# Kernel tuning notes

Hardware: AMD Instinct MI355X
Metric: run time of the kernel (lower is better)

## Reference

```python
import jax, jax.numpy as jnp
import numpy as np

B, T, I, H, L, S = 128, 256, 256, 256, 4, 3


def _gru(x_t, w_i, b_i, b_h):
    # torch.nn.GRUCell called WITHOUT hx in the source => hidden state is 0,
    # so Whh @ 0 vanishes and only the b_hh bias contributes to the gates.
    gi = x_t @ w_i.T + b_i                      # [B, 3H]
    hh = b_h.shape[0] // 3
    i_r, i_z, i_n = gi[:, :hh], gi[:, hh:2 * hh], gi[:, 2 * hh:]
    h_r, h_z, h_n = b_h[:hh], b_h[hh:2 * hh], b_h[2 * hh:]
    r = jax.nn.sigmoid(i_r + h_r)
    z = jax.nn.sigmoid(i_z + h_z)
    n = jnp.tanh(i_n + r * h_n)
    return (1.0 - z) * n                        # + z * 0


def setup_inputs() -> dict:
    key = jax.random.key(0)
    ks = jax.random.split(key, 12)
    s = 1.0 / np.sqrt(H)
    u = lambda k, shape: jax.random.uniform(k, shape, jnp.float32, -s, s)
    return {
        "x": jax.random.normal(ks[0], (B, T, I), jnp.float32),
        "hidden": jax.random.normal(ks[1], (B, L, L), jnp.float32),
        "w_ih0": u(ks[2], (S, 3 * H, I)),      # layer-0 input weights, per split
        "b_ih0": u(ks[3], (S, 3 * H)),
        "b_hh0": u(ks[4], (S, 3 * H)),
        "w_ih": u(ks[5], (S, L - 1, 3 * H, H)),  # layers 1..L-1
        "b_ih": u(ks[6], (S, L - 1, 3 * H)),
        "b_hh": u(ks[7], (S, L - 1, 3 * H)),
        "w_lw": u(ks[8], (L, H)),              # layer_weights: Linear(H -> L)
        "b_lw": u(ks[9], (L,)),
        "w_sel": u(ks[10], (S, H + I)),        # selective_layer: Linear(H+I -> S)
        "b_sel": u(ks[11], (S,)),
    }


def reference(x, hidden, w_ih0, b_ih0, b_hh0, w_ih, b_ih, b_hh, w_lw, b_lw, w_sel, b_sel):
    Lm1 = w_ih.shape[1]

    def run_stack(x_t, cur):
        # cur is a (possibly traced) int index selecting one of S GRU stacks
        hs = [_gru(x_t, w_ih0[cur], b_ih0[cur], b_hh0[cur])]
        for l in range(Lm1):
            hs.append(_gru(hs[-1], w_ih[cur, l], b_ih[cur, l], b_hh[cur, l]))
        return jnp.stack(hs, axis=1)            # [B, L, H]

    h0 = run_stack(x[:, 0, :], 0)               # first step always uses stack 0

    def step(h, x_t):
        energy = h @ w_lw.T + b_lw              # [B, L, L]
        attn = jnp.sum(hidden * energy, axis=2) # [B, L]
        a = jax.nn.softmax(attn, axis=1)
        ctx = jnp.einsum('bl,blh->bh', a, h)    # [B, H]
        scores = jnp.concatenate([ctx, x_t], axis=1) @ w_sel.T + b_sel  # [B, S]
        cur = jnp.argmax(jnp.sum(scores, axis=0))  # batch-summed routing
        h_new = run_stack(x_t, cur)
        return h_new, h_new[:, -1, :]

    h_final, ys = jax.lax.scan(step, h0, jnp.swapaxes(x[:, 1:, :], 0, 1))
    outputs = jnp.concatenate([h0[:, -1:, :], jnp.swapaxes(ys, 0, 1)], axis=1)  # [B, T, H]
    return outputs, h_final[:, -1, :]
```

## Files before the change

### kernel.cpp

```cpp
#include <hip/hip_runtime.h>
#include <math.h>

#define Bsz 128
#define Tsz 256
#define Isz 256
#define Hsz 256
#define Lsz 4
#define Ssz 3
#define Mrows (Bsz*Tsz)

using f16x8 = __attribute__((ext_vector_type(8))) _Float16;
using f32x4 = __attribute__((ext_vector_type(4))) float;

#define LOG2E 1.44269504f

__global__ __launch_bounds__(256) void f32_to_f16_3(
    const float* __restrict__ s0, _Float16* __restrict__ d0, int n0,
    const float* __restrict__ s1, _Float16* __restrict__ d1, int n1,
    const float* __restrict__ s2, _Float16* __restrict__ d2, int n2)
{
  int idx = blockIdx.x * 256 + threadIdx.x;
  const float* s; _Float16* d;
  if (idx < n0)           { s = s0; d = d0; }
  else if (idx < n0 + n1) { idx -= n0; s = s1; d = d1; }
  else                    { idx -= n0 + n1; if (idx >= n2) return; s = s2; d = d2; }
  const float4 v0 = *(const float4*)(s + (size_t)idx * 8);
  const float4 v1 = *(const float4*)(s + (size_t)idx * 8 + 4);
  _Float16 h[8];
  h[0] = (_Float16)v0.x; h[1] = (_Float16)v0.y;
  h[2] = (_Float16)v0.z; h[3] = (_Float16)v0.w;
  h[4] = (_Float16)v1.x; h[5] = (_Float16)v1.y;
  h[6] = (_Float16)v1.z; h[7] = (_Float16)v1.w;
  *(uint4*)(d + (size_t)idx * 8) = *(uint4*)h;
}

__global__ __launch_bounds__(256, 2) void gemm_gru_f16(
    const _Float16* __restrict__ Abase, size_t a_cur_stride,
    const _Float16* __restrict__ Wbase, size_t w_cur_stride,
    const float* __restrict__ bi_g, size_t bi_stride,
    const float* __restrict__ bh_g, size_t bh_stride,
    _Float16* __restrict__ Hout)
{
  __shared__ _Float16 AhS[3][8192];

  const int tid  = threadIdx.x;
  const int cu   = blockIdx.z;
  const int n0   = blockIdx.y * 64;
  const int rmb  = blockIdx.x * 256;

  const _Float16* A = Abase + (size_t)cu * a_cur_stride;
  const _Float16* W = Wbase + (size_t)cu * w_cur_stride;
  const float* bi = bi_g + (size_t)cu * bi_stride;
  const float* bh = bh_g + (size_t)cu * bh_stride;

  const int lane = tid & 63;
  const int wv   = tid >> 6;
  const int q    = lane >> 4;
  const int c    = lane & 15;

  const int ncol = n0 + wv * 16 + c;
  f16x8 wf[3][8];
  #pragma unroll
  for (int s = 0; s < 3; s++)
    #pragma unroll
    for (int k0 = 0; k0 < 8; k0++)
      wf[s][k0] = *(const f16x8*)(W + (size_t)(s * 256 + ncol) * 256 + k0 * 32 + q * 8);
  #pragma unroll
  for (int s = 0; s < 3; s++)
    #pragma unroll
    for (int k0 = 0; k0 < 8; k0++)
      asm volatile("" : "+v"(wf[s][k0]));

  const float c0  = -LOG2E * (bi[ncol] + bh[ncol]);
  const float c1  =  LOG2E * (bi[256 + ncol] + bh[256 + ncol]);
  const float c3  = 2.f * LOG2E * bi[512 + ncol];
  const float bhn = bh[512 + ncol];

  f32x4 acc[3][2];

  auto stage = [&](int buf, int ch) {
    const int rm = rmb + ch * 32;
    #pragma unroll
    for (int i = 0; i < 4; i++) {
      const int p0 = 8 * wv + 2 * i;
      const int pk = p0 + (lane >> 5);
      const _Float16* src = A + (size_t)(rm + (lane & 31)) * 256 + pk * 8;
      __builtin_amdgcn_global_load_lds(
          (const __attribute__((address_space(1))) void*)src,
          (__attribute__((address_space(3))) void*)&AhS[buf][p0 * 256],
          16, 0, 0);
    }
  };

  auto compute_chunk = [&](int buf, int ch) {
    const int rm = rmb + ch * 32;
    #pragma unroll
    for (int s = 0; s < 3; s++)
      #pragma unroll
      for (int mi = 0; mi < 2; mi++)
        acc[s][mi] = (f32x4)0.f;
    #pragma unroll
    for (int k0 = 0; k0 < 8; k0++) {
      const f16x8 a0 = *(const f16x8*)&AhS[buf][(k0 * 4 + q) * 256 + c * 8];
      const f16x8 a1 = *(const f16x8*)&AhS[buf][(k0 * 4 + q) * 256 + 128 + c * 8];
      #pragma unroll
      for (int s = 0; s < 3; s++) {
        acc[s][0] = __builtin_amdgcn_mfma_f32_16x16x32_f16(a0, wf[s][k0], acc[s][0], 0, 0, 0);
        acc[s][1] = __builtin_amdgcn_mfma_f32_16x16x32_f16(a1, wf[s][k0], acc[s][1], 0, 0, 0);
      }
    }
    #pragma unroll
    for (int mi = 0; mi < 2; mi++) {
      #pragma unroll
      for (int reg = 0; reg < 4; reg++) {
        const float ar = acc[0][mi][reg];
        const float az = acc[1][mi][reg];
        const float an = acc[2][mi][reg];
        const float e0 = __builtin_amdgcn_exp2f(fmaf(-LOG2E, ar, c0));
        const float r  = __builtin_amdgcn_rcpf(1.f + e0);
        const float e1 = __builtin_amdgcn_exp2f(fmaf(LOG2E, az, c1));
        const float tt = fmaf(r, bhn, an);
        const float a2 = fminf(fmaf(2.f * LOG2E, tt, c3), 120.f);
        const float e2 = __builtin_amdgcn_exp2f(a2);
        const float out = (e2 - 1.f) *
            __builtin_amdgcn_rcpf((1.f + e1) * (1.f + e2));
        const size_t row = (size_t)cu * Mrows + rm + mi * 16 + q * 4 + reg;
        Hout[row * 256 + ncol] = (_Float16)out;
      }
    }
  };

  stage(0, 0);
  stage(1, 1);
  asm volatile("s_waitcnt vmcnt(4)" ::: "memory");
  __builtin_amdgcn_s_barrier();

  int bc = 0;
  for (int t = 0; t < 6; ++t) {
    int bs = bc + 2; if (bs >= 3) bs -= 3;
    stage(bs, t + 2);
    compute_chunk(bc, t);
    asm volatile("s_waitcnt vmcnt(12)" ::: "memory");
    __builtin_amdgcn_s_barrier();
    bc = (bc + 1 == 3) ? 0 : bc + 1;
  }
  compute_chunk(bc, 6);
  asm volatile("s_waitcnt vmcnt(0)" ::: "memory");
  __builtin_amdgcn_s_barrier();
  compute_chunk(1, 7);
}

__global__ __launch_bounds__(256) void ep_tile(
    const _Float16* __restrict__ Hh,
    const float* __restrict__ w_lw, const float* __restrict__ w_sel, int layer,
    float* __restrict__ e, float* __restrict__ p)
{
  __shared__ float wc[7][256];
  __shared__ float ps[4][64][8];
  const int tid = threadIdx.x;
  const size_t mg0 = (size_t)blockIdx.x * 64;

  #pragma unroll
  for (int j = 0; j < 7; j++)
    wc[j][tid] = (j < 4) ? w_lw[j * 256 + tid] : w_sel[(j - 4) * 512 + tid];
  __syncthreads();

  const int r = tid & 63, pp = tid >> 6;
  const _Float16* hrow = Hh + (mg0 + r) * 256 + pp * 64;
  float acc[7] = {0.f, 0.f, 0.f, 0.f, 0.f, 0.f, 0.f};
  #pragma unroll
  for (int i = 0; i < 8; i++) {
    union { uint4 u; _Float16 h[8]; } hv;
    hv.u = *(const uint4*)(hrow + i * 8);
    float hf[8];
    #pragma unroll
    for (int k = 0; k < 8; k++) hf[k] = (float)hv.h[k];
    #pragma unroll
    for (int j = 0; j < 7; j++) {
      const float4 w0 = *(const float4*)&wc[j][pp * 64 + i * 8];
      const float4 w1 = *(const float4*)&wc[j][pp * 64 + i * 8 + 4];
      acc[j] += hf[0] * w0.x + hf[1] * w0.y + hf[2] * w0.z + hf[3] * w0.w
              + hf[4] * w1.x + hf[5] * w1.y + hf[6] * w1.z + hf[7] * w1.w;
    }
  }
  #pragma unroll
  for (int j = 0; j < 7; j++) ps[pp][r][j] = acc[j];
  __syncthreads();

  if (tid < 64) {
    float d[7];
    #pragma unroll
    for (int j = 0; j < 7; j++)
      d[j] = ps[0][tid][j] + ps[1][tid][j] + ps[2][tid][j] + ps[3][tid][j];
    const size_t mg = mg0 + tid;
    const int cc = (int)(mg >> 15);
    const int m  = (int)(mg & 32767);
    const int b = m >> 8, t = m & 255;
    const size_t base = ((size_t)cc * Tsz + t) * Bsz + b;
    #pragma unroll
    for (int j = 0; j < 4; j++) e[base * 16 + layer * 4 + j] = d[j];
    #pragma unroll
    for (int j = 0; j < 3; j++) p[base * 12 + layer * 3 + j] = d[4 + j];
  }
}

__global__ __launch_bounds__(128) void attn_finish(
    const float* __restrict__ e, const float* __restrict__ p,
    const float* __restrict__ hidden, const float* __restrict__ b_lw,
    float* __restrict__ score_h)
{
  const int t = blockIdx.x, cc = blockIdx.y;
  const int b = threadIdx.x;
  const float* eb = e + ((size_t)(cc * Tsz + t) * Bsz + b) * 16;
  const float* pb = p + ((size_t)(cc * Tsz + t) * Bsz + b) * 12;
  const float* hb = hidden + b * 16;
  const float bl0 = b_lw[0], bl1 = b_lw[1], bl2 = b_lw[2], bl3 = b_lw[3];
  float attn[4];
  #pragma unroll
  for (int i = 0; i < 4; i++) {
    attn[i] = hb[i * 4 + 0] * (eb[i * 4 + 0] + bl0)
            + hb[i * 4 + 1] * (eb[i * 4 + 1] + bl1)
            + hb[i * 4 + 2] * (eb[i * 4 + 2] + bl2)
            + hb[i * 4 + 3] * (eb[i * 4 + 3] + bl3);
  }
  const float mx = fmaxf(fmaxf(attn[0], attn[1]), fmaxf(attn[2], attn[3]));
  float ex[4], sum = 0.f;
  #pragma unroll
  for (int i = 0; i < 4; i++) { ex[i] = expf(attn[i] - mx); sum += ex[i]; }
  const float inv = 1.f / sum;
  float sc[3];
  #pragma unroll
  for (int s = 0; s < 3; s++) {
    float v = 0.f;
    #pragma unroll
    for (int i = 0; i < 4; i++) v += ex[i] * pb[i * 3 + s];
    sc[s] = v * inv;
  }
  #pragma unroll
  for (int off = 32; off; off >>= 1)
    #pragma unroll
    for (int s = 0; s < 3; s++) sc[s] += __shfl_xor(sc[s], off);
  __shared__ float red[2][3];
  const int wv = threadIdx.x >> 6, ln = threadIdx.x & 63;
  if (ln == 0) { red[wv][0] = sc[0]; red[wv][1] = sc[1]; red[wv][2] = sc[2]; }
  __syncthreads();
  if (threadIdx.x == 0) {
    #pragma unroll
    for (int s = 0; s < 3; s++)
      score_h[((size_t)cc * Tsz + t) * 3 + s] = red[0][s] + red[1][s];
  }
}

__global__ __launch_bounds__(256) void xs_kernel(
    const float* __restrict__ x, const float* __restrict__ w_sel,
    const float* __restrict__ b_sel, float* __restrict__ xs)
{
  const int t = blockIdx.x, k = threadIdx.x;
  float s = 0.f;
  for (int b = 0; b < Bsz; b++) s += x[((size_t)b * Tsz + t) * Isz + k];
  float pr[3];
  #pragma unroll
  for (int qq = 0; qq < 3; qq++) pr[qq] = s * w_sel[qq * (Hsz + Isz) + Hsz + k];
  #pragma unroll
  for (int off = 32; off; off >>= 1)
    #pragma unroll
    for (int qq = 0; qq < 3; qq++) pr[qq] += __shfl_xor(pr[qq], off);
  __shared__ float red[4][3];
  const int wv = k >> 6, ln = k & 63;
  if (ln == 0) { red[wv][0] = pr[0]; red[wv][1] = pr[1]; red[wv][2] = pr[2]; }
  __syncthreads();
  if (k == 0) {
    #pragma unroll
    for (int qq = 0; qq < 3; qq++)
      xs[t * 3 + qq] = red[0][qq] + red[1][qq] + red[2][qq] + red[3][qq]
                      + (float)Bsz * b_sel[qq];
  }
}

__global__ __launch_bounds__(256) void select_kernel(
    const float* __restrict__ score_h, const float* __restrict__ xs,
    int* __restrict__ cur)
{
  __shared__ unsigned S[Tsz];
  const int t = threadIdx.x;

  unsigned m = 0x24;
  if (t >= 1) {
    m = 0;
    const float* xr = xs + t * 3;
    #pragma unroll
    for (int cc = 0; cc < 3; cc++) {
      const float* sh = score_h + ((size_t)cc * Tsz + (t - 1)) * 3;
      const float v0 = sh[0] + xr[0];
      const float v1 = sh[1] + xr[1];
      const float v2 = sh[2] + xr[2];
      unsigned best = 0; float bv = v0;
      if (v1 > bv) { bv = v1; best = 1; }
      if (v2 > bv) { bv = v2; best = 2; }
      m |= best << (2 * cc);
    }
  }
  S[t] = m;
  __syncthreads();

  #pragma unroll
  for (int d = 1; d < Tsz; d <<= 1) {
    const unsigned prev = (t >= d) ? S[t - d] : 0x24u;
    const unsigned self = S[t];
    __syncthreads();
    unsigned comp = 0;
    #pragma unroll
    for (int x = 0; x < 3; x++) {
      const unsigned y = (prev >> (2 * x)) & 3u;
      const unsigned z = (self >> (2 * y)) & 3u;
      comp |= z << (2 * x);
    }
    S[t] = comp;
    __syncthreads();
  }
  cur[t] = (int)(S[t] & 3u);
}

__global__ __launch_bounds__(256) void gather_out(
    const _Float16* __restrict__ Hh, const int* __restrict__ cur,
    float* __restrict__ out)
{
  const size_t idx = ((size_t)blockIdx.x * 256 + threadIdx.x) * 4;
  const size_t BTH = (size_t)Bsz * Tsz * Hsz;
  int b, t, h;
  if (idx < BTH) {
    b = (int)(idx >> 16);
    const int rem = (int)(idx & 65535);
    t = rem >> 8; h = rem & 255;
  } else {
    const size_t r2 = idx - BTH;
    b = (int)(r2 >> 8); h = (int)(r2 & 255); t = Tsz - 1;
  }
  const int cc = cur[t];
  const size_t g = (((size_t)cc * Mrows + (size_t)b * Tsz + t) * Hsz + h);
  union { ushort4 u; _Float16 hv[4]; } cv;
  cv.u = *(const ushort4*)(Hh + g);
  float4 v;
  v.x = (float)cv.hv[0]; v.y = (float)cv.hv[1];
  v.z = (float)cv.hv[2]; v.w = (float)cv.hv[3];
  *(float4*)(out + idx) = v;
}

extern "C" void kernel_launch(void* const* d_in, const int* in_sizes, int n_in,
                              void* d_out, int out_size, void* d_ws, size_t ws_size,
                              hipStream_t stream) {
  const float* x      = (const float*)d_in[0];
  const float* hidden = (const float*)d_in[1];
  const float* w_ih0  = (const float*)d_in[2];
  const float* b_ih0  = (const float*)d_in[3];
  const float* b_hh0  = (const float*)d_in[4];
  const float* w_ih   = (const float*)d_in[5];
  const float* b_ih   = (const float*)d_in[6];
  const float* b_hh   = (const float*)d_in[7];
  const float* w_lw   = (const float*)d_in[8];
  const float* b_lw   = (const float*)d_in[9];
  const float* w_sel  = (const float*)d_in[10];
  const float* b_sel  = (const float*)d_in[11];
  float* out = (float*)d_out;

  char* w = (char*)d_ws;
  const size_t HN = (size_t)3 * Mrows * 256;
  const size_t XN = (size_t)Bsz * Tsz * Isz;
  const size_t W0N = (size_t)3 * 768 * 256;
  const size_t WLN = (size_t)3 * 3 * 768 * 256;
  _Float16* HA  = (_Float16*)w; w += HN * 2;
  _Float16* HB  = (_Float16*)w; w += HN * 2;
  _Float16* xh  = (_Float16*)w; w += XN * 2;
  _Float16* Wh0 = (_Float16*)w; w += W0N * 2;
  _Float16* WhL = (_Float16*)w; w += WLN * 2;
  float* e       = (float*)w; w += (size_t)3 * Tsz * Bsz * 16 * 4;
  float* p       = (float*)w; w += (size_t)3 * Tsz * Bsz * 12 * 4;
  float* score_h = (float*)w; w += (size_t)3 * Tsz * 3 * 4;
  float* xsb     = (float*)w; w += (size_t)Tsz * 3 * 4;
  int*   curb    = (int*)w;   w += (size_t)Tsz * 4;

  f32_to_f16_3<<<5248, 256, 0, stream>>>(
      x, xh, (int)(XN / 8),
      w_ih0, Wh0, (int)(W0N / 8),
      w_ih, WhL, (int)(WLN / 8));

  dim3 ggrid(128, 4, 3);

  gemm_gru_f16<<<ggrid, 256, 0, stream>>>(
      xh, (size_t)0, Wh0, (size_t)768 * 256,
      b_ih0, (size_t)768, b_hh0, (size_t)768, HA);
  ep_tile<<<(3 * Mrows) / 64, 256, 0, stream>>>(HA, w_lw, w_sel, 0, e, p);

  const size_t wcur = (size_t)3 * 768 * 256;
  const size_t bst  = (size_t)3 * 768;
  _Float16* ping = HA; _Float16* pong = HB;
  for (int l = 1; l < 4; l++) {
    gemm_gru_f16<<<ggrid, 256, 0, stream>>>(
        ping, (size_t)Mrows * 256,
        WhL + (size_t)(l - 1) * 768 * 256, wcur,
        b_ih + (size_t)(l - 1) * 768, bst,
        b_hh + (size_t)(l - 1) * 768, bst, pong);
    ep_tile<<<(3 * Mrows) / 64, 256, 0, stream>>>(pong, w_lw, w_sel, l, e, p);
    _Float16* t1 = ping; ping = pong; pong = t1;
  }

  attn_finish<<<dim3(Tsz, 3), 128, 0, stream>>>(e, p, hidden, b_lw, score_h);
  xs_kernel<<<Tsz, 256, 0, stream>>>(x, w_sel, b_sel, xsb);
  select_kernel<<<1, 256, 0, stream>>>(score_h, xsb, curb);
  gather_out<<<8224, 256, 0, stream>>>(ping, curb, out);
}
```

Measured before the change: 417.6 us.

## Double-buffer GRU GEMM accumulators to overlap epilogue with MFMA; merge attn/xs kernels

The GRU GEMM kernel now keeps two accumulator sets, so the sigmoid/tanh epilogue of one 32-row chunk is interleaved with the MFMAs of the next. Each block covers 512 rows (16 chunks), halving the grid and amortising the register-resident weight loads over more work. The attention-finish and x-selection reductions are merged into one launch to save a kernel launch. The extra accumulators raise register pressure, which may cut occupancy under the two-block launch bound, and the smaller grid may leave compute units underused.

```diff
diff --git a/kernel.cpp b/kernel.cpp
--- a/kernel.cpp
+++ b/kernel.cpp
@@ -46,7 +46,7 @@
   const int tid  = threadIdx.x;
   const int cu   = blockIdx.z;
   const int n0   = blockIdx.y * 64;
-  const int rmb  = blockIdx.x * 256;
+  const int rmb  = blockIdx.x * 512;
 
   const _Float16* A = Abase + (size_t)cu * a_cur_stride;
   const _Float16* W = Wbase + (size_t)cu * w_cur_stride;
@@ -76,7 +76,7 @@
   const float c3  = 2.f * LOG2E * bi[512 + ncol];
   const float bhn = bh[512 + ncol];
 
-  f32x4 acc[3][2];
+  f32x4 accA[3][2], accB[3][2];
 
   auto stage = [&](int buf, int ch) {
     const int rm = rmb + ch * 32;
@@ -92,8 +92,7 @@
     }
   };
 
-  auto compute_chunk = [&](int buf, int ch) {
-    const int rm = rmb + ch * 32;
+  auto mfma_chunk = [&](f32x4 (&acc)[3][2], int buf) {
     #pragma unroll
     for (int s = 0; s < 3; s++)
       #pragma unroll
@@ -109,6 +108,10 @@
         acc[s][1] = __builtin_amdgcn_mfma_f32_16x16x32_f16(a1, wf[s][k0], acc[s][1], 0, 0, 0);
       }
     }
+  };
+
+  auto epi_chunk = [&](f32x4 (&acc)[3][2], int ch) {
+    const int rm = rmb + ch * 32;
     #pragma unroll
     for (int mi = 0; mi < 2; mi++) {
       #pragma unroll
@@ -132,22 +135,34 @@
 
   stage(0, 0);
   stage(1, 1);
-  asm volatile("s_waitcnt vmcnt(4)" ::: "memory");
-  __builtin_amdgcn_s_barrier();
-
-  int bc = 0;
-  for (int t = 0; t < 6; ++t) {
-    int bs = bc + 2; if (bs >= 3) bs -= 3;
-    stage(bs, t + 2);
-    compute_chunk(bc, t);
-    asm volatile("s_waitcnt vmcnt(12)" ::: "memory");
-    __builtin_amdgcn_s_barrier();
-    bc = (bc + 1 == 3) ? 0 : bc + 1;
-  }
-  compute_chunk(bc, 6);
   asm volatile("s_waitcnt vmcnt(0)" ::: "memory");
   __builtin_amdgcn_s_barrier();
-  compute_chunk(1, 7);
+
+  for (int tt = 0; tt < 7; ++tt) {
+    const int t0 = 2 * tt;
+    {
+      stage((t0 + 2) % 3, t0 + 2);
+      mfma_chunk(accA, t0 % 3);
+      if (tt > 0) epi_chunk(accB, t0 - 1);
+      asm volatile("s_waitcnt vmcnt(12)" ::: "memory");
+      __builtin_amdgcn_s_barrier();
+    }
+    {
+      const int t1 = t0 + 1;
+      stage((t1 + 2) % 3, t1 + 2);
+      mfma_chunk(accB, t1 % 3);
+      epi_chunk(accA, t0);
+      asm volatile("s_waitcnt vmcnt(12)" ::: "memory");
+      __builtin_amdgcn_s_barrier();
+    }
+  }
+  mfma_chunk(accA, 2);
+  epi_chunk(accB, 13);
+  asm volatile("s_waitcnt vmcnt(0)" ::: "memory");
+  __builtin_amdgcn_s_barrier();
+  mfma_chunk(accB, 0);
+  epi_chunk(accA, 14);
+  epi_chunk(accB, 15);
 }
 
 __global__ __launch_bounds__(256) void ep_tile(
@@ -204,76 +219,79 @@
   }
 }
 
-__global__ __launch_bounds__(128) void attn_finish(
+__global__ __launch_bounds__(128) void attn_xs(
     const float* __restrict__ e, const float* __restrict__ p,
     const float* __restrict__ hidden, const float* __restrict__ b_lw,
-    float* __restrict__ score_h)
-{
-  const int t = blockIdx.x, cc = blockIdx.y;
-  const int b = threadIdx.x;
-  const float* eb = e + ((size_t)(cc * Tsz + t) * Bsz + b) * 16;
-  const float* pb = p + ((size_t)(cc * Tsz + t) * Bsz + b) * 12;
-  const float* hb = hidden + b * 16;
-  const float bl0 = b_lw[0], bl1 = b_lw[1], bl2 = b_lw[2], bl3 = b_lw[3];
-  float attn[4];
-  #pragma unroll
-  for (int i = 0; i < 4; i++) {
-    attn[i] = hb[i * 4 + 0] * (eb[i * 4 + 0] + bl0)
-            + hb[i * 4 + 1] * (eb[i * 4 + 1] + bl1)
-            + hb[i * 4 + 2] * (eb[i * 4 + 2] + bl2)
-            + hb[i * 4 + 3] * (eb[i * 4 + 3] + bl3);
-  }
-  const float mx = fmaxf(fmaxf(attn[0], attn[1]), fmaxf(attn[2], attn[3]));
-  float ex[4], sum = 0.f;
-  #pragma unroll
-  for (int i = 0; i < 4; i++) { ex[i] = expf(attn[i] - mx); sum += ex[i]; }
-  const float inv = 1.f / sum;
-  float sc[3];
-  #pragma unroll
-  for (int s = 0; s < 3; s++) {
-    float v = 0.f;
-    #pragma unroll
-    for (int i = 0; i < 4; i++) v += ex[i] * pb[i * 3 + s];
-    sc[s] = v * inv;
-  }
-  #pragma unroll
-  for (int off = 32; off; off >>= 1)
-    #pragma unroll
-    for (int s = 0; s < 3; s++) sc[s] += __shfl_xor(sc[s], off);
+    const float* __restrict__ x, const float* __restrict__ w_sel,
+    const float* __restrict__ b_sel,
+    float* __restrict__ score_h, float* __restrict__ xs)
+{
   __shared__ float red[2][3];
+  const int t = blockIdx.x;
   const int wv = threadIdx.x >> 6, ln = threadIdx.x & 63;
-  if (ln == 0) { red[wv][0] = sc[0]; red[wv][1] = sc[1]; red[wv][2] = sc[2]; }
-  __syncthreads();
-  if (threadIdx.x == 0) {
-    #pragma unroll
-    for (int s = 0; s < 3; s++)
-      score_h[((size_t)cc * Tsz + t) * 3 + s] = red[0][s] + red[1][s];
-  }
-}
-
-__global__ __launch_bounds__(256) void xs_kernel(
-    const float* __restrict__ x, const float* __restrict__ w_sel,
-    const float* __restrict__ b_sel, float* __restrict__ xs)
-{
-  const int t = blockIdx.x, k = threadIdx.x;
-  float s = 0.f;
-  for (int b = 0; b < Bsz; b++) s += x[((size_t)b * Tsz + t) * Isz + k];
-  float pr[3];
-  #pragma unroll
-  for (int qq = 0; qq < 3; qq++) pr[qq] = s * w_sel[qq * (Hsz + Isz) + Hsz + k];
-  #pragma unroll
-  for (int off = 32; off; off >>= 1)
-    #pragma unroll
-    for (int qq = 0; qq < 3; qq++) pr[qq] += __shfl_xor(pr[qq], off);
-  __shared__ float red[4][3];
-  const int wv = k >> 6, ln = k & 63;
-  if (ln == 0) { red[wv][0] = pr[0]; red[wv][1] = pr[1]; red[wv][2] = pr[2]; }
-  __syncthreads();
-  if (k == 0) {
+
+  if (blockIdx.y < 3) {
+    const int cc = blockIdx.y;
+    const int b = threadIdx.x;
+    const float* eb = e + ((size_t)(cc * Tsz + t) * Bsz + b) * 16;
+    const float* pb = p + ((size_t)(cc * Tsz + t) * Bsz + b) * 12;
+    const float* hb = hidden + b * 16;
+    const float bl0 = b_lw[0], bl1 = b_lw[1], bl2 = b_lw[2], bl3 = b_lw[3];
+    float attn[4];
+    #pragma unroll
+    for (int i = 0; i < 4; i++) {
+      attn[i] = hb[i * 4 + 0] * (eb[i * 4 + 0] + bl0)
+              + hb[i * 4 + 1] * (eb[i * 4 + 1] + bl1)
+              + hb[i * 4 + 2] * (eb[i * 4 + 2] + bl2)
+              + hb[i * 4 + 3] * (eb[i * 4 + 3] + bl3);
+    }
+    const float mx = fmaxf(fmaxf(attn[0], attn[1]), fmaxf(attn[2], attn[3]));
+    float ex[4], sum = 0.f;
+    #pragma unroll
+    for (int i = 0; i < 4; i++) { ex[i] = expf(attn[i] - mx); sum += ex[i]; }
+    const float inv = 1.f / sum;
+    float sc[3];
+    #pragma unroll
+    for (int s = 0; s < 3; s++) {
+      float v = 0.f;
+      #pragma unroll
+      for (int i = 0; i < 4; i++) v += ex[i] * pb[i * 3 + s];
+      sc[s] = v * inv;
+    }
+    #pragma unroll
+    for (int off = 32; off; off >>= 1)
+      #pragma unroll
+      for (int s = 0; s < 3; s++) sc[s] += __shfl_xor(sc[s], off);
+    if (ln == 0) { red[wv][0] = sc[0]; red[wv][1] = sc[1]; red[wv][2] = sc[2]; }
+    __syncthreads();
+    if (threadIdx.x == 0) {
+      #pragma unroll
+      for (int s = 0; s < 3; s++)
+        score_h[((size_t)cc * Tsz + t) * 3 + s] = red[0][s] + red[1][s];
+    }
+  } else {
+    const int k = threadIdx.x;
+    float s0 = 0.f, s1 = 0.f;
+    for (int b = 0; b < Bsz; b++) {
+      const float* xb = x + ((size_t)b * Tsz + t) * Isz;
+      s0 += xb[k]; s1 += xb[k + 128];
+    }
+    float pr[3];
     #pragma unroll
     for (int qq = 0; qq < 3; qq++)
-      xs[t * 3 + qq] = red[0][qq] + red[1][qq] + red[2][qq] + red[3][qq]
-                      + (float)Bsz * b_sel[qq];
+      pr[qq] = s0 * w_sel[qq * (Hsz + Isz) + Hsz + k]
+             + s1 * w_sel[qq * (Hsz + Isz) + Hsz + k + 128];
+    #pragma unroll
+    for (int off = 32; off; off >>= 1)
+      #pragma unroll
+      for (int qq = 0; qq < 3; qq++) pr[qq] += __shfl_xor(pr[qq], off);
+    if (ln == 0) { red[wv][0] = pr[0]; red[wv][1] = pr[1]; red[wv][2] = pr[2]; }
+    __syncthreads();
+    if (threadIdx.x == 0) {
+      #pragma unroll
+      for (int qq = 0; qq < 3; qq++)
+        xs[t * 3 + qq] = red[0][qq] + red[1][qq] + (float)Bsz * b_sel[qq];
+    }
   }
 }
 
@@ -310,10 +328,10 @@
     __syncthreads();
     unsigned comp = 0;
     #pragma unroll
-    for (int x = 0; x < 3; x++) {
-      const unsigned y = (prev >> (2 * x)) & 3u;
+    for (int xx = 0; xx < 3; xx++) {
+      const unsigned y = (prev >> (2 * xx)) & 3u;
       const unsigned z = (self >> (2 * y)) & 3u;
-      comp |= z << (2 * x);
+      comp |= z << (2 * xx);
     }
     S[t] = comp;
     __syncthreads();
@@ -384,7 +402,7 @@
       w_ih0, Wh0, (int)(W0N / 8),
       w_ih, WhL, (int)(WLN / 8));
 
-  dim3 ggrid(128, 4, 3);
+  dim3 ggrid(64, 4, 3);
 
   gemm_gru_f16<<<ggrid, 256, 0, stream>>>(
       xh, (size_t)0, Wh0, (size_t)768 * 256,
@@ -404,8 +422,8 @@
     _Float16* t1 = ping; ping = pong; pong = t1;
   }
 
-  attn_finish<<<dim3(Tsz, 3), 128, 0, stream>>>(e, p, hidden, b_lw, score_h);
-  xs_kernel<<<Tsz, 256, 0, stream>>>(x, w_sel, b_sel, xsb);
+  attn_xs<<<dim3(Tsz, 4), 128, 0, stream>>>(
+      e, p, hidden, b_lw, x, w_sel, b_sel, score_h, xsb);
   select_kernel<<<1, 256, 0, stream>>>(score_h, xsb, curb);
   gather_out<<<8224, 256, 0, stream>>>(ping, curb, out);
 }
```

Result: no change. 412.7 us (-1.2%).
